# Kernel optimization log

Measured on AMD Instinct MI355X. Metric: run time of the kernel, lower is better.

The kernel has to match this reference:

```python
import jax, jax.numpy as jnp
import numpy as np

N_NODES = 20000
N_EDGES = 640000
HIDDEN = 128


def setup_inputs() -> dict:
    key = jax.random.key(0)
    k1, k2, k3, k4 = jax.random.split(key, 4)
    scale = 1.0 / np.sqrt(HIDDEN)
    features = jax.random.normal(k1, (N_NODES, HIDDEN), dtype=jnp.float32)
    edge_index = jax.random.randint(k2, (2, N_EDGES), 0, N_NODES, dtype=jnp.int64)
    W_l = jax.random.normal(k3, (HIDDEN, HIDDEN), dtype=jnp.float32) * scale
    b_l = jnp.zeros((HIDDEN,), dtype=jnp.float32)
    W_r = jax.random.normal(k4, (HIDDEN, HIDDEN), dtype=jnp.float32) * scale
    return {"features": features, "edge_index": edge_index, "W_l": W_l, "b_l": b_l, "W_r": W_r}


def reference(features, edge_index, W_l, b_l, W_r):
    # PyG SAGEConv with mean aggregation:
    #   out_i = lin_l(mean_{j : (j->i) in E} x_j) + lin_r(x_i)
    # edge_index[0] = source nodes, edge_index[1] = target nodes.
    n = features.shape[0]
    src = edge_index[0]
    dst = edge_index[1]
    msg = features[src]  # [E, d] gather
    summed = jax.ops.segment_sum(msg, dst, num_segments=n)  # [N, d] scatter-add
    cnt = jax.ops.segment_sum(jnp.ones(src.shape[0], dtype=features.dtype), dst, num_segments=n)
    agg = summed / jnp.maximum(cnt, 1.0)[:, None]  # mean; isolated nodes -> 0
    return agg @ W_l.T + b_l + features @ W_r.T
```

## Files before the change

### kernel.cpp

```cpp
#include <hip/hip_runtime.h>

#define N_NODES 20000
#define N_EDGES 640000
#define HIDDEN  128
#define CAP     96
#define DEG_PAD 16

typedef unsigned short bf16_t;
typedef __attribute__((ext_vector_type(8))) short short8;
typedef __attribute__((ext_vector_type(8))) unsigned short ushort8_t;
typedef __attribute__((ext_vector_type(4))) float floatx4;

__device__ __forceinline__ bf16_t f2bf(float f) {
    union { float f; unsigned int i; } v; v.f = f;
    unsigned int x = v.i + 0x7FFFu + ((v.i >> 16) & 1u);
    return (bf16_t)(x >> 16);
}
__device__ __forceinline__ float bflo(unsigned u) {
    union { unsigned i; float f; } v; v.i = u << 16; return v.f;
}
__device__ __forceinline__ float bfhi(unsigned u) {
    union { unsigned i; float f; } v; v.i = u & 0xFFFF0000u; return v.f;
}

__global__ __launch_bounds__(256) void prep_fill_kernel(
        const float* __restrict__ feat,
        const float* __restrict__ Wl,
        const float* __restrict__ Wr,
        const int* __restrict__ eidx,
        bf16_t* __restrict__ feat_bf,
        bf16_t* __restrict__ Bp,
        int* __restrict__ deg,
        unsigned short* __restrict__ bucket) {
    int t = blockIdx.x * 256 + threadIdx.x;
    float4 v = ((const float4*)feat)[t];
    ushort4 o = { f2bf(v.x), f2bf(v.y), f2bf(v.z), f2bf(v.w) };
    ((ushort4*)feat_bf)[t] = o;
    int src = eidx[t];
    int dst = eidx[N_EDGES + t];
    int pos = atomicAdd(&deg[dst * DEG_PAD], 1);
    if (pos < CAP) bucket[dst * CAP + pos] = (unsigned short)src;
    if (t < 2 * HIDDEN * HIDDEN) {
        int j    = t & 7;
        int lane = (t >> 3) & 63;
        int nt   = (t >> 9) & 15;
        int kt   = t >> 13;
        int n = nt * 16 + (lane & 15);
        int k = kt * 32 + (lane >> 4) * 8 + j;
        float w = (n < HIDDEN) ? Wl[n * HIDDEN + k] : Wr[(n - HIDDEN) * HIDDEN + k];
        Bp[t] = f2bf(w);
    }
}

__global__ __launch_bounds__(256) void gemm_kernel(
        const bf16_t* __restrict__ feat_bf,
        const bf16_t* __restrict__ Bp,
        const float* __restrict__ bl,
        bf16_t* __restrict__ Y,
        float* __restrict__ Z) {
    int wid = blockIdx.x * 4 + (threadIdx.x >> 6);
    if (wid >= N_NODES / 16) return;
    int lane = threadIdx.x & 63;
    int m    = lane & 15;
    int quad = lane >> 4;
    int row0 = wid * 16;

    floatx4 acc[16];
    floatx4 zf = {0.f, 0.f, 0.f, 0.f};
#pragma unroll
    for (int nt = 0; nt < 16; ++nt) acc[nt] = zf;

    const short8* bp = (const short8*)Bp;
#pragma unroll
    for (int kt = 0; kt < 4; ++kt) {
        short8 afrag = *(const short8*)(feat_bf + (size_t)(row0 + m) * HIDDEN
                                        + kt * 32 + quad * 8);
#pragma unroll
        for (int nt = 0; nt < 16; ++nt) {
            short8 bfrag = bp[(kt * 16 + nt) * 64 + lane];
            acc[nt] = __builtin_amdgcn_mfma_f32_16x16x32_bf16(afrag, bfrag, acc[nt], 0, 0, 0);
        }
    }
    int col = lane & 15;
#pragma unroll
    for (int nt = 0; nt < 8; ++nt) {
#pragma unroll
        for (int r = 0; r < 4; ++r) {
            int row = row0 + quad * 4 + r;
            Y[(size_t)row * HIDDEN + nt * 16 + col] = f2bf(acc[nt][r]);
        }
    }
#pragma unroll
    for (int nt = 8; nt < 16; ++nt) {
        float b = bl[(nt - 8) * 16 + col];
#pragma unroll
        for (int r = 0; r < 4; ++r) {
            int row = row0 + quad * 4 + r;
            Z[(size_t)row * HIDDEN + (nt - 8) * 16 + col] = acc[nt][r] + b;
        }
    }
}

__global__ __launch_bounds__(256) void gather_final_kernel(
        const bf16_t* __restrict__ Y,
        const float* __restrict__ Z,
        const int* __restrict__ deg,
        const unsigned short* __restrict__ bucket,
        float* __restrict__ out) {
    int wid  = (blockIdx.x * 256 + threadIdx.x) >> 6;
    int lane = threadIdx.x & 63;
    if (wid >= N_NODES) return;
    int d_true = deg[wid * DEG_PAD];
    int d = min(d_true, CAP);
    const unsigned short* row = bucket + wid * CAP;
    const unsigned* y = (const unsigned*)Y;
    float ax0=0,ay0=0, ax1=0,ay1=0, ax2=0,ay2=0, ax3=0,ay3=0;
    int i = 0;
    for (; i + 16 <= d; i += 16) {
        ushort8_t s0 = *(const ushort8_t*)(row + i);
        ushort8_t s1 = *(const ushort8_t*)(row + i + 8);
        unsigned u0 = y[(int)s0[0] * 64 + lane];
        unsigned u1 = y[(int)s0[1] * 64 + lane];
        unsigned u2 = y[(int)s0[2] * 64 + lane];
        unsigned u3 = y[(int)s0[3] * 64 + lane];
        unsigned u4 = y[(int)s0[4] * 64 + lane];
        unsigned u5 = y[(int)s0[5] * 64 + lane];
        unsigned u6 = y[(int)s0[6] * 64 + lane];
        unsigned u7 = y[(int)s0[7] * 64 + lane];
        unsigned w0 = y[(int)s1[0] * 64 + lane];
        unsigned w1 = y[(int)s1[1] * 64 + lane];
        unsigned w2 = y[(int)s1[2] * 64 + lane];
        unsigned w3 = y[(int)s1[3] * 64 + lane];
        unsigned w4 = y[(int)s1[4] * 64 + lane];
        unsigned w5 = y[(int)s1[5] * 64 + lane];
        unsigned w6 = y[(int)s1[6] * 64 + lane];
        unsigned w7 = y[(int)s1[7] * 64 + lane];
        ax0 += bflo(u0); ay0 += bfhi(u0);
        ax1 += bflo(u1); ay1 += bfhi(u1);
        ax2 += bflo(u2); ay2 += bfhi(u2);
        ax3 += bflo(u3); ay3 += bfhi(u3);
        ax0 += bflo(u4); ay0 += bfhi(u4);
        ax1 += bflo(u5); ay1 += bfhi(u5);
        ax2 += bflo(u6); ay2 += bfhi(u6);
        ax3 += bflo(u7); ay3 += bfhi(u7);
        ax0 += bflo(w0); ay0 += bfhi(w0);
        ax1 += bflo(w1); ay1 += bfhi(w1);
        ax2 += bflo(w2); ay2 += bfhi(w2);
        ax3 += bflo(w3); ay3 += bfhi(w3);
        ax0 += bflo(w4); ay0 += bfhi(w4);
        ax1 += bflo(w5); ay1 += bfhi(w5);
        ax2 += bflo(w6); ay2 += bfhi(w6);
        ax3 += bflo(w7); ay3 += bfhi(w7);
    }
    for (; i + 8 <= d; i += 8) {
        ushort8_t s = *(const ushort8_t*)(row + i);
        unsigned u0 = y[(int)s[0] * 64 + lane];
        unsigned u1 = y[(int)s[1] * 64 + lane];
        unsigned u2 = y[(int)s[2] * 64 + lane];
        unsigned u3 = y[(int)s[3] * 64 + lane];
        unsigned u4 = y[(int)s[4] * 64 + lane];
        unsigned u5 = y[(int)s[5] * 64 + lane];
        unsigned u6 = y[(int)s[6] * 64 + lane];
        unsigned u7 = y[(int)s[7] * 64 + lane];
        ax0 += bflo(u0); ay0 += bfhi(u0);
        ax1 += bflo(u1); ay1 += bfhi(u1);
        ax2 += bflo(u2); ay2 += bfhi(u2);
        ax3 += bflo(u3); ay3 += bfhi(u3);
        ax0 += bflo(u4); ay0 += bfhi(u4);
        ax1 += bflo(u5); ay1 += bfhi(u5);
        ax2 += bflo(u6); ay2 += bfhi(u6);
        ax3 += bflo(u7); ay3 += bfhi(u7);
    }
    for (; i < d; ++i) {
        unsigned u = y[(int)row[i] * 64 + lane];
        ax0 += bflo(u); ay0 += bfhi(u);
    }
    float inv = 1.0f / fmaxf((float)d_true, 1.0f);
    float2 z = ((const float2*)Z)[wid * 64 + lane];
    float2 r;
    r.x = (ax0 + ax1 + ax2 + ax3) * inv + z.x;
    r.y = (ay0 + ay1 + ay2 + ay3) * inv + z.y;
    ((float2*)out)[wid * 64 + lane] = r;
}

extern "C" void kernel_launch(void* const* d_in, const int* in_sizes, int n_in,
                              void* d_out, int out_size, void* d_ws, size_t ws_size,
                              hipStream_t stream) {
    const float* feat = (const float*)d_in[0];
    const int*   eidx = (const int*)d_in[1];
    const float* Wl   = (const float*)d_in[2];
    const float* bl   = (const float*)d_in[3];
    const float* Wr   = (const float*)d_in[4];
    float* out = (float*)d_out;

    int*            deg     = (int*)d_ws;
    unsigned short* bucket  = (unsigned short*)(deg + N_NODES * DEG_PAD);
    bf16_t*         Bp      = (bf16_t*)(bucket + (size_t)N_NODES * CAP);
    bf16_t*         feat_bf = Bp + 2 * HIDDEN * HIDDEN;
    bf16_t*         Y       = feat_bf + (size_t)N_NODES * HIDDEN;
    float*          Z       = (float*)(Y + (size_t)N_NODES * HIDDEN);

    hipMemsetAsync(deg, 0, (size_t)N_NODES * DEG_PAD * sizeof(int), stream);

    prep_fill_kernel<<<N_EDGES / 256, 256, 0, stream>>>(
        feat, Wl, Wr, eidx, feat_bf, Bp, deg, bucket);
    gemm_kernel<<<(N_NODES / 16 + 3) / 4, 256, 0, stream>>>(feat_bf, Bp, bl, Y, Z);
    gather_final_kernel<<<(N_NODES * 64) / 256, 256, 0, stream>>>(Y, Z, deg, bucket, out);
}
```

Baseline: 132.5 us.

## Aggregate raw features first, then apply one concatenated GEMM

Changes the order from transform-then-aggregate to aggregate-then-transform. The gather now averages bf16 input features into a bf16 agg buffer, and a single GEMM over K=256 ([agg | x] times [W_l; W_r]) writes the final output with bias. This drops the fp32 Z intermediate write and read and the separate epilogue pass. In exchange the mean is rounded to bf16 before the matmul, which adds a little precision loss.

```diff
diff --git a/kernel.cpp b/kernel.cpp
--- a/kernel.cpp
+++ b/kernel.cpp
@@ -43,77 +43,27 @@
     if (t < 2 * HIDDEN * HIDDEN) {
         int j    = t & 7;
         int lane = (t >> 3) & 63;
-        int nt   = (t >> 9) & 15;
-        int kt   = t >> 13;
+        int nt   = (t >> 9) & 7;
+        int kt   = t >> 12;
         int n = nt * 16 + (lane & 15);
         int k = kt * 32 + (lane >> 4) * 8 + j;
-        float w = (n < HIDDEN) ? Wl[n * HIDDEN + k] : Wr[(n - HIDDEN) * HIDDEN + k];
+        float w = (k < HIDDEN) ? Wl[n * HIDDEN + k] : Wr[n * HIDDEN + (k - HIDDEN)];
         Bp[t] = f2bf(w);
     }
 }
 
-__global__ __launch_bounds__(256) void gemm_kernel(
+__global__ __launch_bounds__(256) void agg_kernel(
         const bf16_t* __restrict__ feat_bf,
-        const bf16_t* __restrict__ Bp,
-        const float* __restrict__ bl,
-        bf16_t* __restrict__ Y,
-        float* __restrict__ Z) {
-    int wid = blockIdx.x * 4 + (threadIdx.x >> 6);
-    if (wid >= N_NODES / 16) return;
-    int lane = threadIdx.x & 63;
-    int m    = lane & 15;
-    int quad = lane >> 4;
-    int row0 = wid * 16;
-
-    floatx4 acc[16];
-    floatx4 zf = {0.f, 0.f, 0.f, 0.f};
-#pragma unroll
-    for (int nt = 0; nt < 16; ++nt) acc[nt] = zf;
-
-    const short8* bp = (const short8*)Bp;
-#pragma unroll
-    for (int kt = 0; kt < 4; ++kt) {
-        short8 afrag = *(const short8*)(feat_bf + (size_t)(row0 + m) * HIDDEN
-                                        + kt * 32 + quad * 8);
-#pragma unroll
-        for (int nt = 0; nt < 16; ++nt) {
-            short8 bfrag = bp[(kt * 16 + nt) * 64 + lane];
-            acc[nt] = __builtin_amdgcn_mfma_f32_16x16x32_bf16(afrag, bfrag, acc[nt], 0, 0, 0);
-        }
-    }
-    int col = lane & 15;
-#pragma unroll
-    for (int nt = 0; nt < 8; ++nt) {
-#pragma unroll
-        for (int r = 0; r < 4; ++r) {
-            int row = row0 + quad * 4 + r;
-            Y[(size_t)row * HIDDEN + nt * 16 + col] = f2bf(acc[nt][r]);
-        }
-    }
-#pragma unroll
-    for (int nt = 8; nt < 16; ++nt) {
-        float b = bl[(nt - 8) * 16 + col];
-#pragma unroll
-        for (int r = 0; r < 4; ++r) {
-            int row = row0 + quad * 4 + r;
-            Z[(size_t)row * HIDDEN + (nt - 8) * 16 + col] = acc[nt][r] + b;
-        }
-    }
-}
-
-__global__ __launch_bounds__(256) void gather_final_kernel(
-        const bf16_t* __restrict__ Y,
-        const float* __restrict__ Z,
         const int* __restrict__ deg,
         const unsigned short* __restrict__ bucket,
-        float* __restrict__ out) {
+        bf16_t* __restrict__ agg) {
     int wid  = (blockIdx.x * 256 + threadIdx.x) >> 6;
     int lane = threadIdx.x & 63;
     if (wid >= N_NODES) return;
     int d_true = deg[wid * DEG_PAD];
     int d = min(d_true, CAP);
     const unsigned short* row = bucket + wid * CAP;
-    const unsigned* y = (const unsigned*)Y;
+    const unsigned* y = (const unsigned*)feat_bf;
     float ax0=0,ay0=0, ax1=0,ay1=0, ax2=0,ay2=0, ax3=0,ay3=0;
     int i = 0;
     for (; i + 16 <= d; i += 16) {
@@ -176,11 +126,53 @@
         ax0 += bflo(u); ay0 += bfhi(u);
     }
     float inv = 1.0f / fmaxf((float)d_true, 1.0f);
-    float2 z = ((const float2*)Z)[wid * 64 + lane];
-    float2 r;
-    r.x = (ax0 + ax1 + ax2 + ax3) * inv + z.x;
-    r.y = (ay0 + ay1 + ay2 + ay3) * inv + z.y;
-    ((float2*)out)[wid * 64 + lane] = r;
+    float sx = (ax0 + ax1 + ax2 + ax3) * inv;
+    float sy = (ay0 + ay1 + ay2 + ay3) * inv;
+    unsigned pk = (unsigned)f2bf(sx) | ((unsigned)f2bf(sy) << 16);
+    ((unsigned*)agg)[wid * 64 + lane] = pk;
+}
+
+__global__ __launch_bounds__(256) void gemm_out_kernel(
+        const bf16_t* __restrict__ agg,
+        const bf16_t* __restrict__ feat_bf,
+        const bf16_t* __restrict__ Bp,
+        const float* __restrict__ bl,
+        float* __restrict__ out) {
+    int wid = blockIdx.x * 4 + (threadIdx.x >> 6);
+    if (wid >= N_NODES / 16) return;
+    int lane = threadIdx.x & 63;
+    int m    = lane & 15;
+    int quad = lane >> 4;
+    int row0 = wid * 16;
+
+    floatx4 acc[8];
+    floatx4 zf = {0.f, 0.f, 0.f, 0.f};
+#pragma unroll
+    for (int nt = 0; nt < 8; ++nt) acc[nt] = zf;
+
+    const short8* bp = (const short8*)Bp;
+#pragma unroll
+    for (int kt = 0; kt < 8; ++kt) {
+        const bf16_t* abase = (kt < 4)
+            ? (agg     + (size_t)(row0 + m) * HIDDEN + kt * 32 + quad * 8)
+            : (feat_bf + (size_t)(row0 + m) * HIDDEN + (kt - 4) * 32 + quad * 8);
+        short8 afrag = *(const short8*)abase;
+#pragma unroll
+        for (int nt = 0; nt < 8; ++nt) {
+            short8 bfrag = bp[(kt * 8 + nt) * 64 + lane];
+            acc[nt] = __builtin_amdgcn_mfma_f32_16x16x32_bf16(afrag, bfrag, acc[nt], 0, 0, 0);
+        }
+    }
+    int col = lane & 15;
+#pragma unroll
+    for (int nt = 0; nt < 8; ++nt) {
+        float b = bl[nt * 16 + col];
+#pragma unroll
+        for (int r = 0; r < 4; ++r) {
+            int row = row0 + quad * 4 + r;
+            out[(size_t)row * HIDDEN + nt * 16 + col] = acc[nt][r] + b;
+        }
+    }
 }
 
 extern "C" void kernel_launch(void* const* d_in, const int* in_sizes, int n_in,
@@ -197,13 +189,12 @@
     unsigned short* bucket  = (unsigned short*)(deg + N_NODES * DEG_PAD);
     bf16_t*         Bp      = (bf16_t*)(bucket + (size_t)N_NODES * CAP);
     bf16_t*         feat_bf = Bp + 2 * HIDDEN * HIDDEN;
-    bf16_t*         Y       = feat_bf + (size_t)N_NODES * HIDDEN;
-    float*          Z       = (float*)(Y + (size_t)N_NODES * HIDDEN);
+    bf16_t*         agg     = feat_bf + (size_t)N_NODES * HIDDEN;
 
     hipMemsetAsync(deg, 0, (size_t)N_NODES * DEG_PAD * sizeof(int), stream);
 
     prep_fill_kernel<<<N_EDGES / 256, 256, 0, stream>>>(
         feat, Wl, Wr, eidx, feat_bf, Bp, deg, bucket);
-    gemm_kernel<<<(N_NODES / 16 + 3) / 4, 256, 0, stream>>>(feat_bf, Bp, bl, Y, Z);
-    gather_final_kernel<<<(N_NODES * 64) / 256, 256, 0, stream>>>(Y, Z, deg, bucket, out);
-}
+    agg_kernel<<<(N_NODES * 64) / 256, 256, 0, stream>>>(feat_bf, deg, bucket, agg);
+    gemm_out_kernel<<<(N_NODES / 16 + 3) / 4, 256, 0, stream>>>(agg, feat_bf, Bp, bl, out);
+}
```

New measurement: 135.3 us. +2.1%, slower.
